# Kernel tuning notes

Measured on AMD Instinct MI355X. Metric: run time of the kernel, lower is better.

## Reference

```python
import jax, jax.numpy as jnp
import numpy as np

B, T, C = 4, 2048, 1024   # batch, seq (block_size), n_embd
H, D = 16, 64             # num_heads, head_size (H*D == C)


def setup_inputs() -> dict:
    key = jax.random.key(0)
    ks = jax.random.split(key, 6)
    s = 0.02
    return {
        "x":  jax.random.normal(ks[0], (B, T, C), jnp.float32),
        "Wq": jax.random.normal(ks[1], (H, C, D), jnp.float32) * s,
        "Wk": jax.random.normal(ks[2], (H, C, D), jnp.float32) * s,
        "Wv": jax.random.normal(ks[3], (H, C, D), jnp.float32) * s,
        "Wp": jax.random.normal(ks[4], (C, C), jnp.float32) * s,
        "bp": jnp.zeros((C,), jnp.float32),
        "is_masked": 1,
    }


def reference(x, Wq, Wk, Wv, Wp, bp, is_masked):
    # Batched per-head projections (original loops over H separate Linears)
    q = jnp.einsum("btc,hcd->bhtd", x, Wq)
    k = jnp.einsum("btc,hcd->bhtd", x, Wk)
    v = jnp.einsum("btc,hcd->bhtd", x, Wv)
    # NOTE: original divides by sqrt(C) where C = n_embd (input dim), not head_size
    scores = jnp.einsum("bhtd,bhsd->bhts", q, k) / jnp.sqrt(jnp.asarray(C, x.dtype))
    if is_masked:
        causal = jnp.tril(jnp.ones((T, T), bool))
        scores = jnp.where(causal, scores, jnp.asarray(-jnp.inf, scores.dtype))
    attn = jax.nn.softmax(scores, axis=-1)   # dropout is identity in eval mode
    out = jnp.einsum("bhts,bhsd->bhtd", attn, v)
    # concat heads along the last dim: [B,T,H*D] == [B,T,C]
    out = out.transpose(0, 2, 1, 3).reshape(B, T, C)
    return out @ Wp.T + bp
```

## Files before the change

kernel.cpp:

```cpp
#include <hip/hip_runtime.h>
#include <stdint.h>

typedef unsigned short u16;
typedef unsigned int u32;
typedef __attribute__((ext_vector_type(8))) short frag8;
typedef __attribute__((ext_vector_type(4))) float fx4;
typedef __attribute__((ext_vector_type(4))) u32 u32x4;

#define MFMA(a, b, c) __builtin_amdgcn_mfma_f32_16x16x32_bf16((a), (b), (c), 0, 0, 0)

__device__ __forceinline__ void gload16(const void* g, void* l) {
  __builtin_amdgcn_global_load_lds((const __attribute__((address_space(1))) void*)g,
                                   (__attribute__((address_space(3))) void*)l, 16, 0, 0);
}

__device__ __forceinline__ u16 f2bf(float f) {
  union { float f; unsigned int u; } c; c.f = f;
  unsigned int r = c.u + 0x7FFFu + ((c.u >> 16) & 1u);
  return (u16)(r >> 16);
}

__device__ __forceinline__ u32 cvtpk(float lo, float hi) {
  u32 r;
  asm("v_cvt_pk_bf16_f32 %0, %1, %2" : "=v"(r) : "v"(lo), "v"(hi));
  return r;
}


__global__ __launch_bounds__(256) void cvt_x(const float* __restrict__ x, u16* __restrict__ xb) {
  const int n4 = (8192 * 1024) / 4;
  for (int i = blockIdx.x * 256 + threadIdx.x; i < n4; i += 2048 * 256) {
    float4 v = ((const float4*)x)[i];
    ushort4 o;
    o.x = f2bf(v.x); o.y = f2bf(v.y); o.z = f2bf(v.z); o.w = f2bf(v.w);
    ((ushort4*)xb)[i] = o;
  }
}

__global__ __launch_bounds__(256) void cvt_wqkv(const float* __restrict__ Wq,
                                                const float* __restrict__ Wk,
                                                const float* __restrict__ Wv,
                                                u16* __restrict__ Wt) {
  __shared__ u16 Tls[64][72];
  int hh = blockIdx.x;
  int c0 = blockIdx.y * 64;
  int type = hh >> 4, h = hh & 15;
  const float* Wsrc = (type == 0 ? Wq : (type == 1 ? Wk : Wv)) + (size_t)h * 1024 * 64;
  int t = threadIdx.x;
  int cr = t >> 4, q4 = (t & 15) * 4;
  for (int i = 0; i < 4; ++i) {
    int c = cr + i * 16;
    float4 v = *(const float4*)(Wsrc + (size_t)(c0 + c) * 64 + q4);
    Tls[q4 + 0][c] = f2bf(v.x);
    Tls[q4 + 1][c] = f2bf(v.y);
    Tls[q4 + 2][c] = f2bf(v.z);
    Tls[q4 + 3][c] = f2bf(v.w);
  }
  __syncthreads();
  for (int i = 0; i < 4; ++i) {
    int d = cr + i * 16;
    ushort4 o;
    o.x = Tls[d][q4 + 0]; o.y = Tls[d][q4 + 1]; o.z = Tls[d][q4 + 2]; o.w = Tls[d][q4 + 3];
    *(ushort4*)(Wt + ((size_t)hh * 64 + d) * 1024 + c0 + q4) = o;
  }
}

__global__ __launch_bounds__(256) void cvt_wp(const float* __restrict__ Wp, u16* __restrict__ wb) {
  const int n4 = (1024 * 1024) / 4;
  for (int i = blockIdx.x * 256 + threadIdx.x; i < n4; i += 1024 * 256) {
    float4 v = ((const float4*)Wp)[i];
    ushort4 o;
    o.x = f2bf(v.x); o.y = f2bf(v.y); o.z = f2bf(v.z); o.w = f2bf(v.w);
    ((ushort4*)wb)[i] = o;
  }
}

__global__ __launch_bounds__(256) void transpose_v(const u16* __restrict__ Vb, u16* __restrict__ VTg) {
  __shared__ u16 T[64 * 64];
  int bh = blockIdx.x, t0 = blockIdx.y * 64;
  const u16* src = Vb + ((size_t)bh * 2048 + t0) * 64;
  int tid = threadIdx.x;
  int tl = tid >> 2, c16 = (tid & 3) * 16;
  int swzw = (tl & 7) << 4;
  frag8 a = *(const frag8*)(src + (size_t)tl * 64 + c16);
  frag8 b = *(const frag8*)(src + (size_t)tl * 64 + c16 + 8);
  *(frag8*)((char*)T + tl * 128 + ((c16 * 2) ^ swzw)) = a;
  *(frag8*)((char*)T + tl * 128 + ((c16 * 2 + 16) ^ swzw)) = b;
  __syncthreads();
  int d_ = tid & 63;
#pragma unroll
  for (int k = 0; k < 2; ++k) {
    int c_ = (tid >> 6) + 4 * k;
    frag8 o;
#pragma unroll
    for (int j = 0; j < 8; ++j) {
      int t = c_ * 8 + j;
      o[j] = *(const u16*)((const char*)T + t * 128 + ((2 * d_) ^ ((t & 7) << 4)));
    }
    *(frag8*)(VTg + ((size_t)bh * 64 + d_) * 2048 + t0 + c_ * 8) = o;
  }
}


template <int MODE>
__global__ __launch_bounds__(256) void gemm_bt(const u16* __restrict__ A, const u16* __restrict__ Bw,
                                               u16* __restrict__ Qb, u16* __restrict__ Kb,
                                               u16* __restrict__ Vb, float* __restrict__ outp,
                                               const float* __restrict__ bp) {
  __shared__ u16 As[128 * 32];
  __shared__ u16 Bs[128 * 32];
  int tid = threadIdx.x;
  int m0 = blockIdx.x * 128, n0 = blockIdx.y * 128;
  int wid = tid >> 6, lane = tid & 63, lr = lane & 15, lg = lane >> 4;
  int wm = (wid >> 1) * 64, wn = (wid & 1) * 64;
  const u16* Ag = A + (size_t)m0 * 1024;
  const u16* Bg = Bw + (size_t)n0 * 1024;
  int cidx0 = wid * 2, cidx1 = wid * 2 + 1;
  int rA0 = cidx0 * 16 + (lane >> 2), rA1 = cidx1 * 16 + (lane >> 2);
  int chm = ((lane & 3) ^ ((lane >> 2) & 3)) * 8;
  const u16* Asrc0 = Ag + (size_t)rA0 * 1024 + chm;
  const u16* Asrc1 = Ag + (size_t)rA1 * 1024 + chm;
  const u16* Bsrc0 = Bg + (size_t)rA0 * 1024 + chm;
  const u16* Bsrc1 = Bg + (size_t)rA1 * 1024 + chm;
  u16* lA0 = As + cidx0 * 512; u16* lA1 = As + cidx1 * 512;
  u16* lB0 = Bs + cidx0 * 512; u16* lB1 = Bs + cidx1 * 512;
  int aoff[4], boff[4];
#pragma unroll
  for (int i = 0; i < 4; ++i) {
    aoff[i] = (wm + i * 16 + lr) * 64 + ((lg * 16) ^ ((lr & 3) << 4));
    boff[i] = (wn + i * 16 + lr) * 64 + ((lg * 16) ^ ((lr & 3) << 4));
  }
  fx4 acc[4][4] = {};
  for (int kt = 0; kt < 32; ++kt) {
    __syncthreads();
    gload16(Asrc0 + kt * 32, lA0);
    gload16(Asrc1 + kt * 32, lA1);
    gload16(Bsrc0 + kt * 32, lB0);
    gload16(Bsrc1 + kt * 32, lB1);
    __syncthreads();
    frag8 af[4], bf_[4];
#pragma unroll
    for (int i = 0; i < 4; ++i) af[i] = *(const frag8*)((const char*)As + aoff[i]);
#pragma unroll
    for (int i = 0; i < 4; ++i) bf_[i] = *(const frag8*)((const char*)Bs + boff[i]);
#pragma unroll
    for (int mi = 0; mi < 4; ++mi)
#pragma unroll
      for (int ni = 0; ni < 4; ++ni) acc[mi][ni] = MFMA(af[mi], bf_[ni], acc[mi][ni]);
  }
#pragma unroll
  for (int mi = 0; mi < 4; ++mi)
#pragma unroll
    for (int r = 0; r < 4; ++r) {
      int m = m0 + wm + mi * 16 + lg * 4 + r;
      if (MODE == 0) {
        int b = m >> 11, t = m & 2047;
#pragma unroll
        for (int ni = 0; ni < 4; ++ni) {
          int n = n0 + wn + ni * 16 + lr;
          int type = n >> 10, h = (n >> 6) & 15, d = n & 63;
          u16* dst = (type == 0) ? Qb : ((type == 1) ? Kb : Vb);
          dst[((size_t)(b * 16 + h) * 2048 + t) * 64 + d] = f2bf(acc[mi][ni][r]);
        }
      } else {
#pragma unroll
        for (int ni = 0; ni < 4; ++ni) {
          int n = n0 + wn + ni * 16 + lr;
          outp[(size_t)m * 1024 + n] = acc[mi][ni][r] + bp[n];
        }
      }
    }
}


__global__ __launch_bounds__(256) void attn(const u16* __restrict__ Qb, const u16* __restrict__ Kb,
                                            const u16* __restrict__ VTg, u16* __restrict__ Ao,
                                            const int* __restrict__ mflag) {
  __shared__ u16 Ks[64 * 64];
  __shared__ u16 Vs[64 * 64];
  int tid = threadIdx.x, wid = tid >> 6, lane = tid & 63, lr = lane & 15, lg = lane >> 4;
  int bh = blockIdx.x;
  int qt = 31 - (int)blockIdx.y;
  int masked = mflag[0];
  int qbase = qt * 64;
  const u16* Qh = Qb + (size_t)bh * (2048 * 64);
  const u16* Kh = Kb + (size_t)bh * (2048 * 64);
  const u16* Vh = VTg + (size_t)bh * (64 * 2048);
  int qrow = qbase + wid * 16 + lr;
  frag8 qf0 = *(const frag8*)(Qh + (size_t)qrow * 64 + lg * 8);
  frag8 qf1 = *(const frag8*)(Qh + (size_t)qrow * 64 + 32 + lg * 8);
  float m_run = -__builtin_inff(), l_run = 0.f;
  fx4 oacc[4] = {};
  int cidx0 = wid * 2, cidx1 = wid * 2 + 1;
  int rr = lane >> 3, cc8 = ((lane & 7) ^ rr) * 8;
  int krow0 = cidx0 * 8 + rr, krow1 = cidx1 * 8 + rr;
  const u16* kp0 = Kh + (size_t)krow0 * 64 + cc8;
  const u16* kp1 = Kh + (size_t)krow1 * 64 + cc8;
  const u16* vp0 = Vh + (size_t)krow0 * 2048 + cc8;
  const u16* vp1 = Vh + (size_t)krow1 * 2048 + cc8;
  u16* lK0 = Ks + cidx0 * 512; u16* lK1 = Ks + cidx1 * 512;
  u16* lV0 = Vs + cidx0 * 512; u16* lV1 = Vs + cidx1 * 512;
  int ntiles = masked ? (qt + 1) : 32;
  for (int kt = 0; kt < ntiles; ++kt) {
    int s0 = kt * 64;
    __syncthreads();
    gload16(kp0 + (size_t)s0 * 64, lK0);
    gload16(kp1 + (size_t)s0 * 64, lK1);
    gload16(vp0 + s0, lV0);
    gload16(vp1 + s0, lV1);
    __syncthreads();
    fx4 sc[4];
#pragma unroll
    for (int nt = 0; nt < 4; ++nt) {
      int row = nt * 16 + lr, swz = (row & 7) << 4;
      frag8 ka = *(const frag8*)((const char*)Ks + row * 128 + ((lg * 16) ^ swz));
      frag8 kb = *(const frag8*)((const char*)Ks + row * 128 + ((64 + lg * 16) ^ swz));
      fx4 a = {};
      a = MFMA(ka, qf0, a);
      a = MFMA(kb, qf1, a);
      sc[nt] = a;
    }
#pragma unroll
    for (int nt = 0; nt < 4; ++nt)
#pragma unroll
      for (int r = 0; r < 4; ++r) sc[nt][r] *= 0.03125f;
    if (masked && kt == qt) {
      int q_l = wid * 16 + lr;
#pragma unroll
      for (int nt = 0; nt < 4; ++nt)
#pragma unroll
        for (int r = 0; r < 4; ++r)
          if (nt * 16 + lg * 4 + r > q_l) sc[nt][r] = -__builtin_inff();
    }
    float mx = sc[0][0];
#pragma unroll
    for (int nt = 0; nt < 4; ++nt)
#pragma unroll
      for (int r = 0; r < 4; ++r) mx = fmaxf(mx, sc[nt][r]);
    mx = fmaxf(mx, __shfl_xor(mx, 16));
    mx = fmaxf(mx, __shfl_xor(mx, 32));
    float mn = fmaxf(m_run, mx);
    float ps = 0.f;
#pragma unroll
    for (int nt = 0; nt < 4; ++nt)
#pragma unroll
      for (int r = 0; r < 4; ++r) {
        float p = __expf(sc[nt][r] - mn);
        sc[nt][r] = p;
        ps += p;
      }
    ps += __shfl_xor(ps, 16);
    ps += __shfl_xor(ps, 32);
    float al = __expf(m_run - mn);
    m_run = mn;
    l_run = l_run * al + ps;
    float alr[4];
#pragma unroll
    for (int r = 0; r < 4; ++r) alr[r] = __shfl(al, lg * 4 + r);
#pragma unroll
    for (int dt = 0; dt < 4; ++dt)
#pragma unroll
      for (int r = 0; r < 4; ++r) oacc[dt][r] *= alr[r];
    u32 pw[4][2];
#pragma unroll
    for (int nt = 0; nt < 4; ++nt) {
      pw[nt][0] = cvtpk(sc[nt][0], sc[nt][1]);
      pw[nt][1] = cvtpk(sc[nt][2], sc[nt][3]);
    }
    int srcA = ((lg & 1) * 2) * 16 + lr;
    int srcB = srcA + 16;
    bool hisel = (lg >> 1) != 0;
    union { u32x4 u; frag8 f; } P0, P1;
#pragma unroll
    for (int w = 0; w < 4; ++w) {
      int src = (w < 2) ? srcA : srcB;
      int h = w & 1;
      u32 a0 = (u32)__shfl((int)pw[0][h], src);
      u32 a1 = (u32)__shfl((int)pw[1][h], src);
      P0.u[w] = hisel ? a1 : a0;
      u32 b0 = (u32)__shfl((int)pw[2][h], src);
      u32 b1 = (u32)__shfl((int)pw[3][h], src);
      P1.u[w] = hisel ? b1 : b0;
    }
#pragma unroll
    for (int dt = 0; dt < 4; ++dt) {
      int row = dt * 16 + lr, swz = (row & 7) << 4;
      frag8 vf0 = *(const frag8*)((const char*)Vs + row * 128 + ((lg * 16) ^ swz));
      frag8 vf1 = *(const frag8*)((const char*)Vs + row * 128 + ((64 + lg * 16) ^ swz));
      oacc[dt] = MFMA(P0.f, vf0, oacc[dt]);
      oacc[dt] = MFMA(P1.f, vf1, oacc[dt]);
    }
  }
  float inv = 1.0f / l_run;
  float invr[4];
#pragma unroll
  for (int r = 0; r < 4; ++r) invr[r] = __shfl(inv, lg * 4 + r);
  int b = bh >> 4, h = bh & 15;
#pragma unroll
  for (int r = 0; r < 4; ++r) {
    int rowg = qbase + wid * 16 + lg * 4 + r;
    size_t base = ((size_t)b * 2048 + rowg) * 1024 + h * 64;
#pragma unroll
    for (int dt = 0; dt < 4; ++dt) Ao[base + dt * 16 + lr] = f2bf(oacc[dt][r] * invr[r]);
  }
}


extern "C" void kernel_launch(void* const* d_in, const int* in_sizes, int n_in,
                              void* d_out, int out_size, void* d_ws, size_t ws_size,
                              hipStream_t stream) {
  const float* x = (const float*)d_in[0];
  const float* Wq = (const float*)d_in[1];
  const float* Wk = (const float*)d_in[2];
  const float* Wv = (const float*)d_in[3];
  const float* Wp = (const float*)d_in[4];
  const float* bp = (const float*)d_in[5];
  const int* is_masked = (const int*)d_in[6];
  float* out = (float*)d_out;
  char* ws = (char*)d_ws;
  u16* Xbf = (u16*)(ws + 0);
  u16* Wt  = (u16*)(ws + 16777216);
  u16* Wpb = (u16*)(ws + 23068672);
  u16* Qb  = (u16*)(ws + 25165824);
  u16* Kb  = (u16*)(ws + 41943040);
  u16* Vb  = (u16*)(ws + 58720256);
  u16* Ao  = (u16*)(ws + 75497472);
  u16* VTg = Xbf;

  cvt_x<<<2048, 256, 0, stream>>>(x, Xbf);
  cvt_wqkv<<<dim3(48, 16), 256, 0, stream>>>(Wq, Wk, Wv, Wt);
  cvt_wp<<<1024, 256, 0, stream>>>(Wp, Wpb);
  gemm_bt<0><<<dim3(64, 24), 256, 0, stream>>>(Xbf, Wt, Qb, Kb, Vb, nullptr, nullptr);
  transpose_v<<<dim3(64, 32), 256, 0, stream>>>(Vb, VTg);
  attn<<<dim3(64, 32), 256, 0, stream>>>(Qb, Kb, VTg, Ao, is_masked);
  gemm_bt<1><<<dim3(64, 8), 256, 0, stream>>>(Ao, Wpb, nullptr, nullptr, nullptr, out, bp);
}
```

Before: 197.2 us.

## Rewrite attention with 32x32 MFMA, 128-row Q tiles, double-buffered K/V and lazy rescale

```diff
diff --git a/kernel.cpp b/kernel.cpp
--- a/kernel.cpp
+++ b/kernel.cpp
@@ -1,13 +1,15 @@
 #include <hip/hip_runtime.h>
 #include <stdint.h>
+#include <type_traits>
 
 typedef unsigned short u16;
 typedef unsigned int u32;
 typedef __attribute__((ext_vector_type(8))) short frag8;
 typedef __attribute__((ext_vector_type(4))) float fx4;
-typedef __attribute__((ext_vector_type(4))) u32 u32x4;
+typedef __attribute__((ext_vector_type(16))) float fx16;
 
 #define MFMA(a, b, c) __builtin_amdgcn_mfma_f32_16x16x32_bf16((a), (b), (c), 0, 0, 0)
+#define MFMA32(a, b, c) __builtin_amdgcn_mfma_f32_32x32x16_bf16((a), (b), (c), 0, 0, 0)
 
 __device__ __forceinline__ void gload16(const void* g, void* l) {
   __builtin_amdgcn_global_load_lds((const __attribute__((address_space(1))) void*)g,
@@ -160,7 +162,9 @@
           int n = n0 + wn + ni * 16 + lr;
           int type = n >> 10, h = (n >> 6) & 15, d = n & 63;
           u16* dst = (type == 0) ? Qb : ((type == 1) ? Kb : Vb);
-          dst[((size_t)(b * 16 + h) * 2048 + t) * 64 + d] = f2bf(acc[mi][ni][r]);
+          float v = acc[mi][ni][r];
+          if (type == 0) v *= 0.04508422002778011f;
+          dst[((size_t)(b * 16 + h) * 2048 + t) * 64 + d] = f2bf(v);
         }
       } else {
 #pragma unroll
@@ -173,135 +177,142 @@
 }
 
 
-__global__ __launch_bounds__(256) void attn(const u16* __restrict__ Qb, const u16* __restrict__ Kb,
-                                            const u16* __restrict__ VTg, u16* __restrict__ Ao,
-                                            const int* __restrict__ mflag) {
-  __shared__ u16 Ks[64 * 64];
-  __shared__ u16 Vs[64 * 64];
-  int tid = threadIdx.x, wid = tid >> 6, lane = tid & 63, lr = lane & 15, lg = lane >> 4;
-  int bh = blockIdx.x;
-  int qt = 31 - (int)blockIdx.y;
-  int masked = mflag[0];
-  int qbase = qt * 64;
+__global__ __launch_bounds__(256, 4) void attn(const u16* __restrict__ Qb, const u16* __restrict__ Kb,
+                                               const u16* __restrict__ VTg, u16* __restrict__ Ao,
+                                               const int* __restrict__ mflag) {
+  __shared__ __align__(16) char LDS[32768];
+  const int tid = threadIdx.x, w = tid >> 6, lane = tid & 63;
+  const int l31 = lane & 31, hi = lane >> 5;
+  const int bh = blockIdx.x;
+  const int qt = 15 - (int)blockIdx.y;
+  const int masked = mflag[0];
+  const int qbase = qt * 128;
   const u16* Qh = Qb + (size_t)bh * (2048 * 64);
   const u16* Kh = Kb + (size_t)bh * (2048 * 64);
   const u16* Vh = VTg + (size_t)bh * (64 * 2048);
-  int qrow = qbase + wid * 16 + lr;
-  frag8 qf0 = *(const frag8*)(Qh + (size_t)qrow * 64 + lg * 8);
-  frag8 qf1 = *(const frag8*)(Qh + (size_t)qrow * 64 + 32 + lg * 8);
+  const int qrow = qbase + w * 32 + l31;
+  frag8 qf[4];
+#pragma unroll
+  for (int s = 0; s < 4; ++s) qf[s] = *(const frag8*)(Qh + (size_t)qrow * 64 + s * 16 + hi * 8);
+  const int srow = lane >> 3;
+  const int schunk = ((lane & 7) ^ srow) * 8;
+  const int c0 = w * 2, c1 = w * 2 + 1;
+  const u16* kg0 = Kh + (size_t)(c0 * 8 + srow) * 64 + schunk;
+  const u16* kg1 = Kh + (size_t)(c1 * 8 + srow) * 64 + schunk;
+  const u16* vg0 = Vh + (size_t)(c0 * 8 + srow) * 2048 + schunk;
+  const u16* vg1 = Vh + (size_t)(c1 * 8 + srow) * 2048 + schunk;
+  const int aK = l31 * 128 + ((hi * 16) ^ ((l31 & 7) << 4));
+  const int qmax_w = qbase + w * 32 + 31;
+  const int qmin_w = qbase + w * 32;
   float m_run = -__builtin_inff(), l_run = 0.f;
-  fx4 oacc[4] = {};
-  int cidx0 = wid * 2, cidx1 = wid * 2 + 1;
-  int rr = lane >> 3, cc8 = ((lane & 7) ^ rr) * 8;
-  int krow0 = cidx0 * 8 + rr, krow1 = cidx1 * 8 + rr;
-  const u16* kp0 = Kh + (size_t)krow0 * 64 + cc8;
-  const u16* kp1 = Kh + (size_t)krow1 * 64 + cc8;
-  const u16* vp0 = Vh + (size_t)krow0 * 2048 + cc8;
-  const u16* vp1 = Vh + (size_t)krow1 * 2048 + cc8;
-  u16* lK0 = Ks + cidx0 * 512; u16* lK1 = Ks + cidx1 * 512;
-  u16* lV0 = Vs + cidx0 * 512; u16* lV1 = Vs + cidx1 * 512;
-  int ntiles = masked ? (qt + 1) : 32;
-  for (int kt = 0; kt < ntiles; ++kt) {
-    int s0 = kt * 64;
-    __syncthreads();
-    gload16(kp0 + (size_t)s0 * 64, lK0);
-    gload16(kp1 + (size_t)s0 * 64, lK1);
-    gload16(vp0 + s0, lV0);
-    gload16(vp1 + s0, lV1);
-    __syncthreads();
-    fx4 sc[4];
-#pragma unroll
-    for (int nt = 0; nt < 4; ++nt) {
-      int row = nt * 16 + lr, swz = (row & 7) << 4;
-      frag8 ka = *(const frag8*)((const char*)Ks + row * 128 + ((lg * 16) ^ swz));
-      frag8 kb = *(const frag8*)((const char*)Ks + row * 128 + ((64 + lg * 16) ^ swz));
-      fx4 a = {};
-      a = MFMA(ka, qf0, a);
-      a = MFMA(kb, qf1, a);
-      sc[nt] = a;
+  fx16 oa0 = {}, oa1 = {};
+  const int nt = masked ? (2 * qt + 2) : 32;
+
+  auto STAGE = [&](int B, int T) {
+    size_t ko = (size_t)T * 4096, vo = (size_t)T * 64;
+    gload16(kg0 + ko, LDS + B * 8192 + c0 * 1024);
+    gload16(kg1 + ko, LDS + B * 8192 + c1 * 1024);
+    gload16(vg0 + vo, LDS + 16384 + B * 8192 + c0 * 1024);
+    gload16(vg1 + vo, LDS + 16384 + B * 8192 + c1 * 1024);
+  };
+
+  auto TILE = [&](auto Bc, int T) {
+    constexpr int B = decltype(Bc)::value;
+    if (T + 1 < nt) STAGE(B ^ 1, T + 1);
+    bool act = (!masked) || (T * 64 <= qmax_w);
+    if (act) {
+      fx16 s0v = {}, s1v = {};
+#pragma unroll
+      for (int ds = 0; ds < 4; ++ds) {
+        frag8 k0 = *(const frag8*)(LDS + B * 8192 + (aK ^ (ds << 5)));
+        frag8 k1 = *(const frag8*)(LDS + B * 8192 + 4096 + (aK ^ (ds << 5)));
+        s0v = MFMA32(k0, qf[ds], s0v);
+        s1v = MFMA32(k1, qf[ds], s1v);
+      }
+      if (masked && T * 64 + 63 > qmin_w) {
+#pragma unroll
+        for (int g = 0; g < 4; ++g)
+#pragma unroll
+          for (int r = 0; r < 4; ++r) {
+            int sg = T * 64 + r + 8 * g + 4 * hi;
+            if (sg > qrow) s0v[4 * g + r] = -__builtin_inff();
+            if (sg + 32 > qrow) s1v[4 * g + r] = -__builtin_inff();
+          }
+      }
+      float mx = s0v[0];
+#pragma unroll
+      for (int i = 1; i < 16; ++i) mx = fmaxf(mx, s0v[i]);
+#pragma unroll
+      for (int i = 0; i < 16; ++i) mx = fmaxf(mx, s1v[i]);
+      mx = fmaxf(mx, __int_as_float(__shfl_xor(__float_as_int(mx), 32)));
+      if (!__all(mx <= m_run + 8.0f)) {
+        float mn = fmaxf(m_run, mx);
+        float al = __builtin_amdgcn_exp2f(m_run - mn);
+#pragma unroll
+        for (int i = 0; i < 16; ++i) { oa0[i] *= al; oa1[i] *= al; }
+        l_run *= al;
+        m_run = mn;
+      }
+      float ps = 0.f;
+#pragma unroll
+      for (int i = 0; i < 16; ++i) {
+        s0v[i] = __builtin_amdgcn_exp2f(s0v[i] - m_run); ps += s0v[i];
+      }
+#pragma unroll
+      for (int i = 0; i < 16; ++i) {
+        s1v[i] = __builtin_amdgcn_exp2f(s1v[i] - m_run); ps += s1v[i];
+      }
+      ps += __int_as_float(__shfl_xor(__float_as_int(ps), 32));
+      l_run += ps;
+#pragma unroll
+      for (int kt = 0; kt < 4; ++kt) {
+        const int b8 = (kt & 1) * 8;
+        float p0, p1, p2, p3, p4, p5, p6, p7;
+        if (kt < 2) { p0=s0v[b8+0];p1=s0v[b8+1];p2=s0v[b8+2];p3=s0v[b8+3];p4=s0v[b8+4];p5=s0v[b8+5];p6=s0v[b8+6];p7=s0v[b8+7]; }
+        else        { p0=s1v[b8+0];p1=s1v[b8+1];p2=s1v[b8+2];p3=s1v[b8+3];p4=s1v[b8+4];p5=s1v[b8+5];p6=s1v[b8+6];p7=s1v[b8+7]; }
+        u32 X0 = cvtpk(p0, p1), X1 = cvtpk(p2, p3);
+        u32 Y0 = cvtpk(p4, p5), Y1 = cvtpk(p6, p7);
+        u32 sel0 = hi ? X0 : Y0, sel1 = hi ? X1 : Y1;
+        u32 got0 = (u32)__shfl_xor((int)sel0, 32);
+        u32 got1 = (u32)__shfl_xor((int)sel1, 32);
+        union { u32 u[4]; frag8 f; } pf;
+        pf.u[0] = hi ? got0 : X0;
+        pf.u[1] = hi ? got1 : X1;
+        pf.u[2] = hi ? Y0 : got0;
+        pf.u[3] = hi ? Y1 : got1;
+        frag8 v0 = *(const frag8*)(LDS + 16384 + B * 8192 + (aK ^ (kt << 5)));
+        frag8 v1 = *(const frag8*)(LDS + 16384 + B * 8192 + 4096 + (aK ^ (kt << 5)));
+        oa0 = MFMA32(v0, pf.f, oa0);
+        oa1 = MFMA32(v1, pf.f, oa1);
+      }
     }
-#pragma unroll
-    for (int nt = 0; nt < 4; ++nt)
-#pragma unroll
-      for (int r = 0; r < 4; ++r) sc[nt][r] *= 0.03125f;
-    if (masked && kt == qt) {
-      int q_l = wid * 16 + lr;
-#pragma unroll
-      for (int nt = 0; nt < 4; ++nt)
-#pragma unroll
-        for (int r = 0; r < 4; ++r)
-          if (nt * 16 + lg * 4 + r > q_l) sc[nt][r] = -__builtin_inff();
-    }
-    float mx = sc[0][0];
-#pragma unroll
-    for (int nt = 0; nt < 4; ++nt)
-#pragma unroll
-      for (int r = 0; r < 4; ++r) mx = fmaxf(mx, sc[nt][r]);
-    mx = fmaxf(mx, __shfl_xor(mx, 16));
-    mx = fmaxf(mx, __shfl_xor(mx, 32));
-    float mn = fmaxf(m_run, mx);
-    float ps = 0.f;
-#pragma unroll
-    for (int nt = 0; nt < 4; ++nt)
-#pragma unroll
-      for (int r = 0; r < 4; ++r) {
-        float p = __expf(sc[nt][r] - mn);
-        sc[nt][r] = p;
-        ps += p;
-      }
-    ps += __shfl_xor(ps, 16);
-    ps += __shfl_xor(ps, 32);
-    float al = __expf(m_run - mn);
-    m_run = mn;
-    l_run = l_run * al + ps;
-    float alr[4];
-#pragma unroll
-    for (int r = 0; r < 4; ++r) alr[r] = __shfl(al, lg * 4 + r);
-#pragma unroll
-    for (int dt = 0; dt < 4; ++dt)
-#pragma unroll
-      for (int r = 0; r < 4; ++r) oacc[dt][r] *= alr[r];
-    u32 pw[4][2];
-#pragma unroll
-    for (int nt = 0; nt < 4; ++nt) {
-      pw[nt][0] = cvtpk(sc[nt][0], sc[nt][1]);
-      pw[nt][1] = cvtpk(sc[nt][2], sc[nt][3]);
-    }
-    int srcA = ((lg & 1) * 2) * 16 + lr;
-    int srcB = srcA + 16;
-    bool hisel = (lg >> 1) != 0;
-    union { u32x4 u; frag8 f; } P0, P1;
-#pragma unroll
-    for (int w = 0; w < 4; ++w) {
-      int src = (w < 2) ? srcA : srcB;
-      int h = w & 1;
-      u32 a0 = (u32)__shfl((int)pw[0][h], src);
-      u32 a1 = (u32)__shfl((int)pw[1][h], src);
-      P0.u[w] = hisel ? a1 : a0;
-      u32 b0 = (u32)__shfl((int)pw[2][h], src);
-      u32 b1 = (u32)__shfl((int)pw[3][h], src);
-      P1.u[w] = hisel ? b1 : b0;
-    }
-#pragma unroll
-    for (int dt = 0; dt < 4; ++dt) {
-      int row = dt * 16 + lr, swz = (row & 7) << 4;
-      frag8 vf0 = *(const frag8*)((const char*)Vs + row * 128 + ((lg * 16) ^ swz));
-      frag8 vf1 = *(const frag8*)((const char*)Vs + row * 128 + ((64 + lg * 16) ^ swz));
-      oacc[dt] = MFMA(P0.f, vf0, oacc[dt]);
-      oacc[dt] = MFMA(P1.f, vf1, oacc[dt]);
-    }
-  }
+    asm volatile("s_waitcnt vmcnt(0)" ::: "memory");
+    __builtin_amdgcn_s_barrier();
+  };
+
+  STAGE(0, 0);
+  asm volatile("s_waitcnt vmcnt(0)" ::: "memory");
+  __builtin_amdgcn_s_barrier();
+  int t = 0;
+  while (true) {
+    TILE(std::integral_constant<int, 0>{}, t); ++t; if (t >= nt) break;
+    TILE(std::integral_constant<int, 1>{}, t); ++t; if (t >= nt) break;
+  }
+
   float inv = 1.0f / l_run;
-  float invr[4];
-#pragma unroll
-  for (int r = 0; r < 4; ++r) invr[r] = __shfl(inv, lg * 4 + r);
-  int b = bh >> 4, h = bh & 15;
-#pragma unroll
-  for (int r = 0; r < 4; ++r) {
-    int rowg = qbase + wid * 16 + lg * 4 + r;
-    size_t base = ((size_t)b * 2048 + rowg) * 1024 + h * 64;
-#pragma unroll
-    for (int dt = 0; dt < 4; ++dt) Ao[base + dt * 16 + lr] = f2bf(oacc[dt][r] * invr[r]);
+  int b = bh >> 4, hh = bh & 15;
+  u16* orow = Ao + ((size_t)b * 2048 + qrow) * 1024 + hh * 64;
+#pragma unroll
+  for (int g = 0; g < 4; ++g) {
+    int d0 = 8 * g + 4 * hi;
+    u32 wA = cvtpk(oa0[4 * g + 0] * inv, oa0[4 * g + 1] * inv);
+    u32 wB = cvtpk(oa0[4 * g + 2] * inv, oa0[4 * g + 3] * inv);
+    u32 wC = cvtpk(oa1[4 * g + 0] * inv, oa1[4 * g + 1] * inv);
+    u32 wD = cvtpk(oa1[4 * g + 2] * inv, oa1[4 * g + 3] * inv);
+    *(u32*)(orow + d0 + 0) = wA;
+    *(u32*)(orow + d0 + 2) = wB;
+    *(u32*)(orow + d0 + 32) = wC;
+    *(u32*)(orow + d0 + 34) = wD;
   }
 }
 
@@ -332,6 +343,6 @@
   cvt_wp<<<1024, 256, 0, stream>>>(Wp, Wpb);
   gemm_bt<0><<<dim3(64, 24), 256, 0, stream>>>(Xbf, Wt, Qb, Kb, Vb, nullptr, nullptr);
   transpose_v<<<dim3(64, 32), 256, 0, stream>>>(Vb, VTg);
-  attn<<<dim3(64, 32), 256, 0, stream>>>(Qb, Kb, VTg, Ao, is_masked);
+  attn<<<dim3(64, 16), 256, 0, stream>>>(Qb, Kb, VTg, Ao, is_masked);
   gemm_bt<1><<<dim3(64, 8), 256, 0, stream>>>(Ao, Wpb, nullptr, nullptr, nullptr, out, bp);
 }
```

Measured after the change: 168.7 us. -14.5%, faster.
